# Kernel tuning notes

Measured on AMD Instinct MI355X. Metric: run time of the kernel, lower is better.

Reference implementation:

```python
import jax, jax.numpy as jnp
import numpy as np
from jax import lax


def setup_inputs() -> dict:
    key = jax.random.key(0)
    k1, k2, k3 = jax.random.split(key, 3)
    T, C, H, W = 8, 1024, 64, 64
    features = jax.random.normal(k1, (T, C, H, W), dtype=jnp.float32)
    # Single shared depthwise kernel ([Conv3d]*input_dim shares one module/weight)
    dw_weight = jax.random.normal(k2, (1, 1, 3, 3, 3), dtype=jnp.float32)
    # Pointwise 1x1x1 conv weight [out_c, in_c, 1, 1, 1]
    pw_weight = jax.random.normal(k3, (1024, 1024, 1, 1, 1), dtype=jnp.float32) * 0.03
    return {"features": features, "dw_weight": dw_weight, "pw_weight": pw_weight}


def reference(features, dw_weight, pw_weight):
    T, C, H, W = features.shape
    # torch: expand to [1,T,C,H,W] then torch.reshape to [1,C,T,H,W]
    # (a raw row-major reshape, NOT a transpose) -- replicate exactly.
    x = features.reshape(1, C, T, H, W)
    # Depthwise temporal conv: every channel uses the SAME [1,1,3,3,3] kernel
    # (the torch list is the same Conv3d object repeated). Express as one
    # grouped conv with the kernel tiled over channels.
    w_dw = jnp.tile(dw_weight, (C, 1, 1, 1, 1))  # [C,1,3,3,3]
    y = lax.conv_general_dilated(
        x, w_dw,
        window_strides=(1, 1, 1),
        padding=((1, 1), (1, 1), (1, 1)),
        feature_group_count=C,
        dimension_numbers=("NCDHW", "OIDHW", "NCDHW"),
    )  # [1,C,T,H,W]
    # Pointwise 1x1x1 conv: [C,C] channel-mixing GEMM per voxel.
    z = jnp.einsum("oc,bcthw->bothw", pw_weight[:, :, 0, 0, 0], y)
    # torch: reshape back [1,C,T,H,W] -> [1,T,C,H,W], then squeeze batch dim.
    return z.reshape(1, T, C, H, W)[0]
```

## Files before the change

kernel.cpp:

```cpp
#include <hip/hip_runtime.h>
#include <hip/hip_bf16.h>
#include <stdint.h>

typedef __attribute__((ext_vector_type(8))) short s8v;
typedef __attribute__((ext_vector_type(4))) float f4v;

#define T_TOT 8
#define NSP 32768
#define K_TOT 1024
#define M_TOT 1024

__device__ __forceinline__ unsigned short f2bf(float f) {
  unsigned int u = __float_as_uint(f);
  u += 0x7FFF + ((u >> 16) & 1);
  return (unsigned short)(u >> 16);
}

__global__ __launch_bounds__(256) void dw_kernel(const float* __restrict__ X,
                                                 const float* __restrict__ DW,
                                                 unsigned short* __restrict__ Yn) {
  __shared__ float xin[8 * 18 * 64];
  const int tid = threadIdx.x;
  const int hb  = blockIdx.x;
  const int c   = blockIdx.y;
  const int h0  = hb * 16;

  float kw[27];
#pragma unroll
  for (int j = 0; j < 27; ++j) kw[j] = DW[j];

  const float* Xc = X + (size_t)c * NSP;

#pragma unroll
  for (int i = 0; i < 9; ++i) {
    const int f  = tid + i * 256;
    const int r  = f >> 4;
    const int wq = (f & 15) * 4;
    const int t  = r / 18;
    const int hr = r - t * 18;
    const int hg = h0 - 1 + hr;
    const int hc = min(max(hg, 0), 63);
    float4 v = *(const float4*)(Xc + (t * 64 + hc) * 64 + wq);
    if (hg != hc) v = (float4){0.f, 0.f, 0.f, 0.f};
    *(float4*)&xin[r * 64 + wq] = v;
  }
  __syncthreads();

  const int w  = tid & 63;
  const int hq = tid >> 6;
  const int wl = (w == 0)  ? w : w - 1;
  const int wr = (w == 63) ? w : w + 1;
  const float* bC = &xin[(hq * 4) * 64 + w];
  const float* bL = &xin[(hq * 4) * 64 + wl];
  const float* bR = &xin[(hq * 4) * 64 + wr];
  unsigned short* Yb = Yn + (size_t)c * NSP + (h0 + hq * 4) * 64 + w;

  float a0[4], a1[4], a2[4];
#pragma unroll
  for (int j = 0; j < 4; ++j) { a0[j] = 0.f; a1[j] = 0.f; a2[j] = 0.f; }

#pragma unroll
  for (int tp = 0; tp < 8; ++tp) {
    float v[6][3];
#pragma unroll
    for (int rr = 0; rr < 6; ++rr) {
      const int off = (tp * 18 + rr) * 64;
      float xc = bC[off];
      float xl = bL[off];
      float xr = bR[off];
      if (w == 0)  xl = 0.f;
      if (w == 63) xr = 0.f;
      v[rr][0] = xl; v[rr][1] = xc; v[rr][2] = xr;
    }
#pragma unroll
    for (int j = 0; j < 4; ++j)
#pragma unroll
      for (int kh = 0; kh < 3; ++kh)
#pragma unroll
        for (int kd = 0; kd < 3; ++kd) {
          const float xv = v[j + kh][kd];
          if (tp >= 1) a0[j] += kw[(2 * 3 + kh) * 3 + kd] * xv;
          a1[j] += kw[(1 * 3 + kh) * 3 + kd] * xv;
          if (tp <= 6) a2[j] += kw[(0 * 3 + kh) * 3 + kd] * xv;
        }
    if (tp >= 1) {
      unsigned short* yp = Yb + (size_t)(tp - 1) * 4096;
#pragma unroll
      for (int j = 0; j < 4; ++j) yp[j * 64] = f2bf(a0[j]);
    }
#pragma unroll
    for (int j = 0; j < 4; ++j) { a0[j] = a1[j]; a1[j] = a2[j]; a2[j] = 0.f; }
  }
  {
    unsigned short* yp = Yb + (size_t)7 * 4096;
#pragma unroll
    for (int j = 0; j < 4; ++j) yp[j * 64] = f2bf(a0[j]);
  }
}

__global__ __launch_bounds__(256) void tr_kernel(const unsigned short* __restrict__ Yn,
                                                 unsigned short* __restrict__ Yt) {
  __shared__ unsigned short tb[64][68];
  const int tid = threadIdx.x;
  const int n0  = blockIdx.x * 64;
  const int c0  = blockIdx.y * 64;

#pragma unroll
  for (int i = 0; i < 2; ++i) {
    const int cl = (tid >> 3) + i * 32;
    const int n8 = (tid & 7) * 8;
    const uint4 v = *(const uint4*)(Yn + (size_t)(c0 + cl) * NSP + n0 + n8);
    uint2 lo; lo.x = v.x; lo.y = v.y;
    uint2 hi; hi.x = v.z; hi.y = v.w;
    *(uint2*)&tb[cl][n8]     = lo;
    *(uint2*)&tb[cl][n8 + 4] = hi;
  }
  __syncthreads();

  const int nl = tid >> 2;
  const int cq = tid & 3;
#pragma unroll
  for (int i = 0; i < 2; ++i) {
    const int c8 = cq * 8 + i * 32;
    unsigned int p[4];
#pragma unroll
    for (int j = 0; j < 4; ++j) {
      const unsigned int a = tb[c8 + 2 * j][nl];
      const unsigned int b = tb[c8 + 2 * j + 1][nl];
      p[j] = a | (b << 16);
    }
    uint4 o; o.x = p[0]; o.y = p[1]; o.z = p[2]; o.w = p[3];
    *(uint4*)(Yt + (size_t)(n0 + nl) * 1024 + c0 + c8) = o;
  }
}

__global__ __launch_bounds__(256) void castw_kernel(const float* __restrict__ Wf,
                                                    unsigned short* __restrict__ Wb) {
  const int i = (blockIdx.x * 256 + threadIdx.x) * 4;
  float4 v = *(const float4*)&Wf[i];
  ushort4 o;
  o.x = f2bf(v.x); o.y = f2bf(v.y); o.z = f2bf(v.z); o.w = f2bf(v.w);
  *(ushort4*)&Wb[i] = o;
}

__device__ __forceinline__ void gload_lds16(const void* g, void* lds) {
  __builtin_amdgcn_global_load_lds(
      (const __attribute__((address_space(1))) void*)(uintptr_t)g,
      (__attribute__((address_space(3))) void*)(uintptr_t)lds, 16, 0, 0);
}

__global__ __launch_bounds__(512, 2) void gemm8_kernel(const unsigned short* __restrict__ A,
                                                       const unsigned short* __restrict__ B,
                                                       float* __restrict__ C) {
  __shared__ char smem[131072];
  const int tid  = threadIdx.x;
  const int lane = tid & 63;
  const int wid  = tid >> 6;
  const int wm   = wid >> 2, wn = wid & 3;

  const int wg = (int)blockIdx.x;
  const int lg = (wg & 7) * 64 + (wg >> 3);
  const int bm = lg & 3;
  const int bn = lg >> 2;

  f4v acc[8][4];
#pragma unroll
  for (int i = 0; i < 8; ++i)
#pragma unroll
    for (int j = 0; j < 4; ++j) acc[i][j] = (f4v){0.f, 0.f, 0.f, 0.f};

  const int r  = tid >> 2;
  const int kb = (((tid & 3) ^ ((tid >> 3) & 3)) * 8);
  const unsigned short* ga = A + (size_t)(bm * 256 + r) * K_TOT + kb;
  const unsigned short* gb = B + (size_t)(bn * 256 + r) * K_TOT + kb;
  const int stg = wid * 1024;

#define STAGE_KK(nb, tt, kk)                                                  \
  do {                                                                        \
    const int ko = (tt) * 64 + (kk) * 32;                                     \
    char* ab = smem + (nb) + (kk) * 16384 + stg;                              \
    char* bb = smem + (nb) + 32768 + (kk) * 16384 + stg;                      \
    gload_lds16(ga + ko,                 ab);                                 \
    gload_lds16(ga + 128 * K_TOT + ko,   ab + 8192);                          \
    gload_lds16(gb + ko,                 bb);                                 \
    gload_lds16(gb + 128 * K_TOT + ko,   bb + 8192);                          \
  } while (0)

  const int cph  = ((lane >> 4) ^ ((lane >> 1) & 3)) * 8;
  const int arow = wm * 128 + (lane & 15);
  const int brow = wn * 64  + (lane & 15);

#define PHASE(cu, nx, tt, kk, pf)                                             \
  do {                                                                        \
    const unsigned short* Ac = (const unsigned short*)(smem + (cu));          \
    const unsigned short* Bc = (const unsigned short*)(smem + (cu) + 32768);  \
    s8v av[8], bv[4];                                                         \
    _Pragma("unroll")                                                         \
    for (int nf = 0; nf < 4; ++nf)                                            \
      bv[nf] = *(const s8v*)&Bc[(kk) * 8192 + (brow + nf * 16) * 32 + cph];   \
    _Pragma("unroll")                                                         \
    for (int mf = 0; mf < 8; ++mf)                                            \
      av[mf] = *(const s8v*)&Ac[(kk) * 8192 + (arow + mf * 16) * 32 + cph];   \
    if (pf) STAGE_KK(nx, (tt) + 1, kk);                                       \
    __builtin_amdgcn_s_setprio(1);                                            \
    _Pragma("unroll")                                                         \
    for (int mf = 0; mf < 8; ++mf)                                            \
      _Pragma("unroll")                                                       \
      for (int nf = 0; nf < 4; ++nf)                                          \
        acc[mf][nf] = __builtin_amdgcn_mfma_f32_16x16x32_bf16(                \
            av[mf], bv[nf], acc[mf][nf], 0, 0, 0);                            \
    __builtin_amdgcn_s_setprio(0);                                            \
  } while (0)

  STAGE_KK(0, 0, 0);
  STAGE_KK(0, 0, 1);

  for (int t = 0; t < 15; ++t) {
    const int cu = (t & 1) << 16;
    const int nx = cu ^ 65536;
    asm volatile("s_waitcnt vmcnt(4)" ::: "memory");
    __builtin_amdgcn_s_barrier();
    PHASE(cu, nx, t, 0, true);
    asm volatile("s_waitcnt vmcnt(4)" ::: "memory");
    __builtin_amdgcn_s_barrier();
    PHASE(cu, nx, t, 1, true);
  }
  asm volatile("s_waitcnt vmcnt(0)" ::: "memory");
  __builtin_amdgcn_s_barrier();
  PHASE(65536, 0, 15, 0, false);
  PHASE(65536, 0, 15, 1, false);

#undef PHASE
#undef STAGE_KK

  const int rowq = (lane >> 4) * 4;
  const int colq = lane & 15;
#pragma unroll
  for (int mf = 0; mf < 8; ++mf) {
    const int row0 = bm * 256 + wm * 128 + mf * 16 + rowq;
#pragma unroll
    for (int nf = 0; nf < 4; ++nf) {
      const int col = bn * 256 + wn * 64 + nf * 16 + colq;
      float* cp = C + (size_t)row0 * NSP + col;
#pragma unroll
      for (int j = 0; j < 4; ++j) cp[(size_t)j * NSP] = acc[mf][nf][j];
    }
  }
}

__global__ __launch_bounds__(256) void gemm_nmajor_kernel(const unsigned short* __restrict__ A,
                                                          const unsigned short* __restrict__ B,
                                                          float* __restrict__ C) {
  __shared__ unsigned short As[128][32];
  __shared__ unsigned short Bs[128][40];
  const int tid  = threadIdx.x;
  const int lane = tid & 63;
  const int wv   = tid >> 6;
  const int wr   = wv >> 1, wc = wv & 1;
  const int bn   = blockIdx.x, bm = blockIdx.y;
  const int n0   = bn * 128;

  f4v acc[4][4];
#pragma unroll
  for (int i = 0; i < 4; ++i)
#pragma unroll
    for (int j = 0; j < 4; ++j) acc[i][j] = (f4v){0.f, 0.f, 0.f, 0.f};

  const int r  = tid >> 2;
  const int kb = (tid & 3) * 8;
  const unsigned short* ga0 = A + (size_t)(bm * 128 + r) * K_TOT + kb;
  char* ldsA = (char*)(&As[0][0]) + wv * 1024;
  const int nq4 = (tid >> 3) * 4;
  const int kq4 = (tid & 7) * 4;

  for (int kt = 0; kt < K_TOT; kt += 32) {
    __syncthreads();
    gload_lds16(ga0 + kt,               ldsA);
    gload_lds16(ga0 + 64 * K_TOT + kt,  ldsA + 4096);

    const unsigned short* gB = B + (size_t)(kt + kq4) * NSP + n0 + nq4;
    uint2 L0 = *(const uint2*)(gB);
    uint2 L1 = *(const uint2*)(gB + NSP);
    uint2 L2 = *(const uint2*)(gB + 2 * NSP);
    uint2 L3 = *(const uint2*)(gB + 3 * NSP);
    uint2 W0, W1, W2, W3;
    W0.x = (L0.x & 0xFFFFu) | (L1.x << 16);
    W0.y = (L2.x & 0xFFFFu) | (L3.x << 16);
    W1.x = (L0.x >> 16) | (L1.x & 0xFFFF0000u);
    W1.y = (L2.x >> 16) | (L3.x & 0xFFFF0000u);
    W2.x = (L0.y & 0xFFFFu) | (L1.y << 16);
    W2.y = (L2.y & 0xFFFFu) | (L3.y << 16);
    W3.x = (L0.y >> 16) | (L1.y & 0xFFFF0000u);
    W3.y = (L2.y >> 16) | (L3.y & 0xFFFF0000u);
    *(uint2*)&Bs[nq4 + 0][kq4] = W0;
    *(uint2*)&Bs[nq4 + 1][kq4] = W1;
    *(uint2*)&Bs[nq4 + 2][kq4] = W2;
    *(uint2*)&Bs[nq4 + 3][kq4] = W3;
    __syncthreads();

    s8v a[4], b[4];
#pragma unroll
    for (int mf = 0; mf < 4; ++mf)
      a[mf] = *(const s8v*)&As[wr * 64 + mf * 16 + (lane & 15)][(lane >> 4) * 8];
#pragma unroll
    for (int nf = 0; nf < 4; ++nf)
      b[nf] = *(const s8v*)&Bs[wc * 64 + nf * 16 + (lane & 15)][(lane >> 4) * 8];
#pragma unroll
    for (int mf = 0; mf < 4; ++mf)
#pragma unroll
      for (int nf = 0; nf < 4; ++nf)
        acc[mf][nf] = __builtin_amdgcn_mfma_f32_16x16x32_bf16(a[mf], b[nf], acc[mf][nf], 0, 0, 0);
  }

  const int rowq = (lane >> 4) * 4;
  const int colq = lane & 15;
#pragma unroll
  for (int mf = 0; mf < 4; ++mf) {
    const int row0 = bm * 128 + wr * 64 + mf * 16 + rowq;
#pragma unroll
    for (int nf = 0; nf < 4; ++nf) {
      const int col = n0 + wc * 64 + nf * 16 + colq;
      float* cp = C + (size_t)row0 * NSP + col;
#pragma unroll
      for (int j = 0; j < 4; ++j) cp[(size_t)j * NSP] = acc[mf][nf][j];
    }
  }
}

extern "C" void kernel_launch(void* const* d_in, const int* in_sizes, int n_in,
                              void* d_out, int out_size, void* d_ws, size_t ws_size,
                              hipStream_t stream) {
  const float* feat = (const float*)d_in[0];
  const float* dw   = (const float*)d_in[1];
  const float* pw   = (const float*)d_in[2];
  float* out = (float*)d_out;

  const size_t YBYTES = (size_t)K_TOT * NSP * 2;

  if (ws_size >= 2 * YBYTES) {
    unsigned short* Yt = (unsigned short*)d_ws;
    unsigned short* Yn = (unsigned short*)((char*)d_ws + YBYTES);
    unsigned short* Wb = Yn;
    dw_kernel<<<dim3(4, 1024), dim3(256), 0, stream>>>(feat, dw, Yn);
    tr_kernel<<<dim3(512, 16), dim3(256), 0, stream>>>(Yn, Yt);
    castw_kernel<<<dim3(1024), dim3(256), 0, stream>>>(pw, Wb);
    gemm8_kernel<<<dim3(512), dim3(512), 0, stream>>>(Wb, Yt, out);
  } else {
    unsigned short* Yn = (unsigned short*)d_ws;
    unsigned short* Wb = Yn + (size_t)K_TOT * NSP;
    dw_kernel<<<dim3(4, 1024), dim3(256), 0, stream>>>(feat, dw, Yn);
    castw_kernel<<<dim3(1024), dim3(256), 0, stream>>>(pw, Wb);
    gemm_nmajor_kernel<<<dim3(256, 8), dim3(256), 0, stream>>>(Wb, Yn, out);
  }
}
```

Measured before the change: 151.9 us.

## Split GEMM K-step into four interleaved phases with finer-grained A/B prefetch

Restructures the main GEMM loop so each 64-wide K tile runs as four sub-phases of 16 MFMAs, interleaving LDS fragment reads, separate A and B global-to-LDS prefetches, and barriers. It halves the A-fragment registers and spreads the memory traffic more evenly across the compute, aiming to overlap loads with MFMA work better and lower register pressure. The cost is more barriers per iteration and more delicate vmcnt accounting, which could add stalls or race hazards.

Measured after the change: 152.9 us. About the same (+0.6%).

```diff
diff --git a/kernel.cpp b/kernel.cpp
--- a/kernel.cpp
+++ b/kernel.cpp
@@ -175,63 +175,123 @@
   const unsigned short* gb = B + (size_t)(bn * 256 + r) * K_TOT + kb;
   const int stg = wid * 1024;
 
-#define STAGE_KK(nb, tt, kk)                                                  \
+#define STAGE_A(nb, tt, kk)                                                   \
   do {                                                                        \
     const int ko = (tt) * 64 + (kk) * 32;                                     \
     char* ab = smem + (nb) + (kk) * 16384 + stg;                              \
+    gload_lds16(ga + ko,               ab);                                   \
+    gload_lds16(ga + 128 * K_TOT + ko, ab + 8192);                            \
+  } while (0)
+#define STAGE_B(nb, tt, kk)                                                   \
+  do {                                                                        \
+    const int ko = (tt) * 64 + (kk) * 32;                                     \
     char* bb = smem + (nb) + 32768 + (kk) * 16384 + stg;                      \
-    gload_lds16(ga + ko,                 ab);                                 \
-    gload_lds16(ga + 128 * K_TOT + ko,   ab + 8192);                          \
-    gload_lds16(gb + ko,                 bb);                                 \
-    gload_lds16(gb + 128 * K_TOT + ko,   bb + 8192);                          \
+    gload_lds16(gb + ko,               bb);                                   \
+    gload_lds16(gb + 128 * K_TOT + ko, bb + 8192);                            \
   } while (0)
 
   const int cph  = ((lane >> 4) ^ ((lane >> 1) & 3)) * 8;
   const int arow = wm * 128 + (lane & 15);
   const int brow = wn * 64  + (lane & 15);
 
-#define PHASE(cu, nx, tt, kk, pf)                                             \
+#define MFMA16(mbase, kkreg)                                                  \
   do {                                                                        \
-    const unsigned short* Ac = (const unsigned short*)(smem + (cu));          \
-    const unsigned short* Bc = (const unsigned short*)(smem + (cu) + 32768);  \
-    s8v av[8], bv[4];                                                         \
-    _Pragma("unroll")                                                         \
-    for (int nf = 0; nf < 4; ++nf)                                            \
-      bv[nf] = *(const s8v*)&Bc[(kk) * 8192 + (brow + nf * 16) * 32 + cph];   \
-    _Pragma("unroll")                                                         \
-    for (int mf = 0; mf < 8; ++mf)                                            \
-      av[mf] = *(const s8v*)&Ac[(kk) * 8192 + (arow + mf * 16) * 32 + cph];   \
-    if (pf) STAGE_KK(nx, (tt) + 1, kk);                                       \
     __builtin_amdgcn_s_setprio(1);                                            \
     _Pragma("unroll")                                                         \
-    for (int mf = 0; mf < 8; ++mf)                                            \
+    for (int mf = 0; mf < 4; ++mf)                                            \
       _Pragma("unroll")                                                       \
       for (int nf = 0; nf < 4; ++nf)                                          \
-        acc[mf][nf] = __builtin_amdgcn_mfma_f32_16x16x32_bf16(                \
-            av[mf], bv[nf], acc[mf][nf], 0, 0, 0);                            \
+        acc[(mbase) + mf][nf] = __builtin_amdgcn_mfma_f32_16x16x32_bf16(      \
+            av[mf], bv[nf], acc[(mbase) + mf][nf], 0, 0, 0);                  \
     __builtin_amdgcn_s_setprio(0);                                            \
   } while (0)
 
-  STAGE_KK(0, 0, 0);
-  STAGE_KK(0, 0, 1);
+  STAGE_A(0, 0, 0);
+  STAGE_B(0, 0, 0);
+  STAGE_A(0, 0, 1);
+  STAGE_B(0, 0, 1);
+  asm volatile("s_waitcnt vmcnt(4)" ::: "memory");
+  __builtin_amdgcn_s_barrier();
 
   for (int t = 0; t < 15; ++t) {
     const int cu = (t & 1) << 16;
     const int nx = cu ^ 65536;
+    const unsigned short* Ac = (const unsigned short*)(smem + cu);
+    const unsigned short* Bc = (const unsigned short*)(smem + cu + 32768);
+    s8v av[4], bv[4];
+
+#pragma unroll
+    for (int nf = 0; nf < 4; ++nf)
+      bv[nf] = *(const s8v*)&Bc[(brow + nf * 16) * 32 + cph];
+#pragma unroll
+    for (int mf = 0; mf < 4; ++mf)
+      av[mf] = *(const s8v*)&Ac[(arow + mf * 16) * 32 + cph];
+    STAGE_A(nx, t + 1, 0);
+    __builtin_amdgcn_s_barrier();
+    MFMA16(0, 0);
+
+#pragma unroll
+    for (int mf = 0; mf < 4; ++mf)
+      av[mf] = *(const s8v*)&Ac[(arow + (mf + 4) * 16) * 32 + cph];
+    STAGE_B(nx, t + 1, 0);
     asm volatile("s_waitcnt vmcnt(4)" ::: "memory");
     __builtin_amdgcn_s_barrier();
-    PHASE(cu, nx, t, 0, true);
+    MFMA16(4, 0);
+
+#pragma unroll
+    for (int nf = 0; nf < 4; ++nf)
+      bv[nf] = *(const s8v*)&Bc[8192 + (brow + nf * 16) * 32 + cph];
+#pragma unroll
+    for (int mf = 0; mf < 4; ++mf)
+      av[mf] = *(const s8v*)&Ac[8192 + (arow + mf * 16) * 32 + cph];
+    STAGE_A(nx, t + 1, 1);
+    __builtin_amdgcn_s_barrier();
+    MFMA16(0, 1);
+
+#pragma unroll
+    for (int mf = 0; mf < 4; ++mf)
+      av[mf] = *(const s8v*)&Ac[8192 + (arow + (mf + 4) * 16) * 32 + cph];
+    STAGE_B(nx, t + 1, 1);
     asm volatile("s_waitcnt vmcnt(4)" ::: "memory");
     __builtin_amdgcn_s_barrier();
-    PHASE(cu, nx, t, 1, true);
-  }
-  asm volatile("s_waitcnt vmcnt(0)" ::: "memory");
-  __builtin_amdgcn_s_barrier();
-  PHASE(65536, 0, 15, 0, false);
-  PHASE(65536, 0, 15, 1, false);
-
-#undef PHASE
-#undef STAGE_KK
+    MFMA16(4, 1);
+  }
+
+  {
+    const unsigned short* Ac = (const unsigned short*)(smem + 65536);
+    const unsigned short* Bc = (const unsigned short*)(smem + 65536 + 32768);
+    s8v av[4], bv[4];
+#pragma unroll
+    for (int nf = 0; nf < 4; ++nf)
+      bv[nf] = *(const s8v*)&Bc[(brow + nf * 16) * 32 + cph];
+#pragma unroll
+    for (int mf = 0; mf < 4; ++mf)
+      av[mf] = *(const s8v*)&Ac[(arow + mf * 16) * 32 + cph];
+    __builtin_amdgcn_s_barrier();
+    MFMA16(0, 0);
+#pragma unroll
+    for (int mf = 0; mf < 4; ++mf)
+      av[mf] = *(const s8v*)&Ac[(arow + (mf + 4) * 16) * 32 + cph];
+    asm volatile("s_waitcnt vmcnt(0)" ::: "memory");
+    __builtin_amdgcn_s_barrier();
+    MFMA16(4, 0);
+#pragma unroll
+    for (int nf = 0; nf < 4; ++nf)
+      bv[nf] = *(const s8v*)&Bc[8192 + (brow + nf * 16) * 32 + cph];
+#pragma unroll
+    for (int mf = 0; mf < 4; ++mf)
+      av[mf] = *(const s8v*)&Ac[8192 + (arow + mf * 16) * 32 + cph];
+    __builtin_amdgcn_s_barrier();
+    MFMA16(0, 1);
+#pragma unroll
+    for (int mf = 0; mf < 4; ++mf)
+      av[mf] = *(const s8v*)&Ac[8192 + (arow + (mf + 4) * 16) * 32 + cph];
+    MFMA16(4, 1);
+  }
+
+#undef MFMA16
+#undef STAGE_A
+#undef STAGE_B
 
   const int rowq = (lane >> 4) * 4;
   const int colq = lane & 15;
```

## Fuse transpose and weight cast into depthwise kernel with 8-channel interleaved layout

Applied to the files above, without the earlier changes.

The depthwise conv kernel now handles 8 channels per block and writes its output as 8-channel bf16 chunks per spatial position (a channel-group-major layout), so the separate transpose kernel is dropped. The weight cast is folded into extra blocks of the same launch. The GEMM B loads are re-addressed to read 16-byte chunks from the new layout. This removes a full read/write pass over the 64MB intermediate and two kernel launches. In exchange, the depthwise kernel has a large register footprint (held[8][4][4]) and only 512 blocks, which may lower occupancy.

Measured after the change: 149.8 us. No clear change (-1.4%).

```diff
diff --git a/kernel.cpp b/kernel.cpp
--- a/kernel.cpp
+++ b/kernel.cpp
@@ -16,35 +16,33 @@
   return (unsigned short)(u >> 16);
 }
 
-__global__ __launch_bounds__(256) void dw_kernel(const float* __restrict__ X,
-                                                 const float* __restrict__ DW,
-                                                 unsigned short* __restrict__ Yn) {
+__global__ __launch_bounds__(256, 2) void dw3_kernel(const float* __restrict__ X,
+                                                     const float* __restrict__ DW,
+                                                     unsigned short* __restrict__ Yn8,
+                                                     const float* __restrict__ Wf,
+                                                     unsigned short* __restrict__ Wb) {
+  if (blockIdx.x == 4) {
+    const int base = blockIdx.y * 8192;
+#pragma unroll
+    for (int it = 0; it < 8; ++it) {
+      const int i = base + (it * 256 + (int)threadIdx.x) * 4;
+      float4 v = *(const float4*)&Wf[i];
+      ushort4 o;
+      o.x = f2bf(v.x); o.y = f2bf(v.y); o.z = f2bf(v.z); o.w = f2bf(v.w);
+      *(ushort4*)&Wb[i] = o;
+    }
+    return;
+  }
+
   __shared__ float xin[8 * 18 * 64];
   const int tid = threadIdx.x;
   const int hb  = blockIdx.x;
-  const int c   = blockIdx.y;
+  const int cg  = blockIdx.y;
   const int h0  = hb * 16;
 
   float kw[27];
 #pragma unroll
   for (int j = 0; j < 27; ++j) kw[j] = DW[j];
-
-  const float* Xc = X + (size_t)c * NSP;
-
-#pragma unroll
-  for (int i = 0; i < 9; ++i) {
-    const int f  = tid + i * 256;
-    const int r  = f >> 4;
-    const int wq = (f & 15) * 4;
-    const int t  = r / 18;
-    const int hr = r - t * 18;
-    const int hg = h0 - 1 + hr;
-    const int hc = min(max(hg, 0), 63);
-    float4 v = *(const float4*)(Xc + (t * 64 + hc) * 64 + wq);
-    if (hg != hc) v = (float4){0.f, 0.f, 0.f, 0.f};
-    *(float4*)&xin[r * 64 + wq] = v;
-  }
-  __syncthreads();
 
   const int w  = tid & 63;
   const int hq = tid >> 6;
@@ -53,94 +51,90 @@
   const float* bC = &xin[(hq * 4) * 64 + w];
   const float* bL = &xin[(hq * 4) * 64 + wl];
   const float* bR = &xin[(hq * 4) * 64 + wr];
-  unsigned short* Yb = Yn + (size_t)c * NSP + (h0 + hq * 4) * 64 + w;
-
-  float a0[4], a1[4], a2[4];
-#pragma unroll
-  for (int j = 0; j < 4; ++j) { a0[j] = 0.f; a1[j] = 0.f; a2[j] = 0.f; }
-
-#pragma unroll
-  for (int tp = 0; tp < 8; ++tp) {
-    float v[6][3];
-#pragma unroll
-    for (int rr = 0; rr < 6; ++rr) {
-      const int off = (tp * 18 + rr) * 64;
-      float xc = bC[off];
-      float xl = bL[off];
-      float xr = bR[off];
-      if (w == 0)  xl = 0.f;
-      if (w == 63) xr = 0.f;
-      v[rr][0] = xl; v[rr][1] = xc; v[rr][2] = xr;
-    }
-#pragma unroll
-    for (int j = 0; j < 4; ++j)
-#pragma unroll
-      for (int kh = 0; kh < 3; ++kh)
-#pragma unroll
-        for (int kd = 0; kd < 3; ++kd) {
-          const float xv = v[j + kh][kd];
-          if (tp >= 1) a0[j] += kw[(2 * 3 + kh) * 3 + kd] * xv;
-          a1[j] += kw[(1 * 3 + kh) * 3 + kd] * xv;
-          if (tp <= 6) a2[j] += kw[(0 * 3 + kh) * 3 + kd] * xv;
+
+  unsigned int held[8][4][4];
+
+#pragma unroll
+  for (int c = 0; c < 8; ++c) {
+    const float* Xc = X + (size_t)(cg * 8 + c) * NSP;
+
+#pragma unroll
+    for (int i = 0; i < 9; ++i) {
+      const int f  = tid + i * 256;
+      const int r  = f >> 4;
+      const int wq = (f & 15) * 4;
+      const int t  = r / 18;
+      const int hr = r - t * 18;
+      const int hg = h0 - 1 + hr;
+      const int hc = min(max(hg, 0), 63);
+      float4 v = *(const float4*)(Xc + (t * 64 + hc) * 64 + wq);
+      if (hg != hc) v = (float4){0.f, 0.f, 0.f, 0.f};
+      *(float4*)&xin[r * 64 + wq] = v;
+    }
+    __syncthreads();
+
+    float a0[4], a1[4], a2[4];
+#pragma unroll
+    for (int j = 0; j < 4; ++j) { a0[j] = 0.f; a1[j] = 0.f; a2[j] = 0.f; }
+
+#pragma unroll
+    for (int tp = 0; tp < 8; ++tp) {
+      float v[6][3];
+#pragma unroll
+      for (int rr = 0; rr < 6; ++rr) {
+        const int off = (tp * 18 + rr) * 64;
+        float xc = bC[off];
+        float xl = bL[off];
+        float xr = bR[off];
+        if (w == 0)  xl = 0.f;
+        if (w == 63) xr = 0.f;
+        v[rr][0] = xl; v[rr][1] = xc; v[rr][2] = xr;
+      }
+#pragma unroll
+      for (int j = 0; j < 4; ++j)
+#pragma unroll
+        for (int kh = 0; kh < 3; ++kh)
+#pragma unroll
+          for (int kd = 0; kd < 3; ++kd) {
+            const float xv = v[j + kh][kd];
+            if (tp >= 1) a0[j] += kw[(2 * 3 + kh) * 3 + kd] * xv;
+            a1[j] += kw[(1 * 3 + kh) * 3 + kd] * xv;
+            if (tp <= 6) a2[j] += kw[(0 * 3 + kh) * 3 + kd] * xv;
+          }
+      if (tp >= 1) {
+        const int to = tp - 1;
+#pragma unroll
+        for (int j = 0; j < 4; ++j) {
+          const unsigned int b = f2bf(a0[j]);
+          if (c & 1) held[to][j][c >> 1] |= (b << 16);
+          else       held[to][j][c >> 1] = b;
         }
-    if (tp >= 1) {
-      unsigned short* yp = Yb + (size_t)(tp - 1) * 4096;
-#pragma unroll
-      for (int j = 0; j < 4; ++j) yp[j * 64] = f2bf(a0[j]);
-    }
-#pragma unroll
-    for (int j = 0; j < 4; ++j) { a0[j] = a1[j]; a1[j] = a2[j]; a2[j] = 0.f; }
-  }
-  {
-    unsigned short* yp = Yb + (size_t)7 * 4096;
-#pragma unroll
-    for (int j = 0; j < 4; ++j) yp[j * 64] = f2bf(a0[j]);
-  }
-}
-
-__global__ __launch_bounds__(256) void tr_kernel(const unsigned short* __restrict__ Yn,
-                                                 unsigned short* __restrict__ Yt) {
-  __shared__ unsigned short tb[64][68];
-  const int tid = threadIdx.x;
-  const int n0  = blockIdx.x * 64;
-  const int c0  = blockIdx.y * 64;
-
-#pragma unroll
-  for (int i = 0; i < 2; ++i) {
-    const int cl = (tid >> 3) + i * 32;
-    const int n8 = (tid & 7) * 8;
-    const uint4 v = *(const uint4*)(Yn + (size_t)(c0 + cl) * NSP + n0 + n8);
-    uint2 lo; lo.x = v.x; lo.y = v.y;
-    uint2 hi; hi.x = v.z; hi.y = v.w;
-    *(uint2*)&tb[cl][n8]     = lo;
-    *(uint2*)&tb[cl][n8 + 4] = hi;
-  }
-  __syncthreads();
-
-  const int nl = tid >> 2;
-  const int cq = tid & 3;
-#pragma unroll
-  for (int i = 0; i < 2; ++i) {
-    const int c8 = cq * 8 + i * 32;
-    unsigned int p[4];
+      }
+#pragma unroll
+      for (int j = 0; j < 4; ++j) { a0[j] = a1[j]; a1[j] = a2[j]; a2[j] = 0.f; }
+    }
+    {
+#pragma unroll
+      for (int j = 0; j < 4; ++j) {
+        const unsigned int b = f2bf(a0[j]);
+        if (c & 1) held[7][j][c >> 1] |= (b << 16);
+        else       held[7][j][c >> 1] = b;
+      }
+    }
+    __syncthreads();
+  }
+
+  const size_t nb = (size_t)cg * NSP;
+#pragma unroll
+  for (int t = 0; t < 8; ++t)
 #pragma unroll
     for (int j = 0; j < 4; ++j) {
-      const unsigned int a = tb[c8 + 2 * j][nl];
-      const unsigned int b = tb[c8 + 2 * j + 1][nl];
-      p[j] = a | (b << 16);
-    }
-    uint4 o; o.x = p[0]; o.y = p[1]; o.z = p[2]; o.w = p[3];
-    *(uint4*)(Yt + (size_t)(n0 + nl) * 1024 + c0 + c8) = o;
-  }
-}
-
-__global__ __launch_bounds__(256) void castw_kernel(const float* __restrict__ Wf,
-                                                    unsigned short* __restrict__ Wb) {
-  const int i = (blockIdx.x * 256 + threadIdx.x) * 4;
-  float4 v = *(const float4*)&Wf[i];
-  ushort4 o;
-  o.x = f2bf(v.x); o.y = f2bf(v.y); o.z = f2bf(v.z); o.w = f2bf(v.w);
-  *(ushort4*)&Wb[i] = o;
+      const int n = t * 4096 + (h0 + hq * 4 + j) * 64 + w;
+      uint4 o;
+      o.x = held[t][j][0]; o.y = held[t][j][1];
+      o.z = held[t][j][2]; o.w = held[t][j][3];
+      *(uint4*)&Yn8[(nb + (size_t)n) * 8] = o;
+    }
 }
 
 __device__ __forceinline__ void gload_lds16(const void* g, void* lds) {
@@ -150,7 +144,7 @@
 }
 
 __global__ __launch_bounds__(512, 2) void gemm8_kernel(const unsigned short* __restrict__ A,
-                                                       const unsigned short* __restrict__ B,
+                                                       const unsigned short* __restrict__ Yn8,
                                                        float* __restrict__ C) {
   __shared__ char smem[131072];
   const int tid  = threadIdx.x;
@@ -169,21 +163,22 @@
 #pragma unroll
     for (int j = 0; j < 4; ++j) acc[i][j] = (f4v){0.f, 0.f, 0.f, 0.f};
 
-  const int r  = tid >> 2;
-  const int kb = (((tid & 3) ^ ((tid >> 3) & 3)) * 8);
-  const unsigned short* ga = A + (size_t)(bm * 256 + r) * K_TOT + kb;
-  const unsigned short* gb = B + (size_t)(bn * 256 + r) * K_TOT + kb;
+  const int r    = tid >> 2;
+  const int cswz = (tid & 3) ^ ((tid >> 3) & 3);
+  const unsigned short* ga  = A + (size_t)(bm * 256 + r) * K_TOT + cswz * 8;
+  const unsigned short* gbb = Yn8 + ((size_t)cswz * NSP + (size_t)(bn * 256 + r)) * 8;
   const int stg = wid * 1024;
 
 #define STAGE_KK(nb, tt, kk)                                                  \
   do {                                                                        \
     const int ko = (tt) * 64 + (kk) * 32;                                     \
+    const size_t bko = (size_t)((tt) * 8 + (kk) * 4) * NSP * 8;               \
     char* ab = smem + (nb) + (kk) * 16384 + stg;                              \
     char* bb = smem + (nb) + 32768 + (kk) * 16384 + stg;                      \
     gload_lds16(ga + ko,                 ab);                                 \
     gload_lds16(ga + 128 * K_TOT + ko,   ab + 8192);                          \
-    gload_lds16(gb + ko,                 bb);                                 \
-    gload_lds16(gb + 128 * K_TOT + ko,   bb + 8192);                          \
+    gload_lds16(gbb + bko,               bb);                                 \
+    gload_lds16(gbb + bko + 128 * 8,     bb + 8192);                          \
   } while (0)
 
   const int cph  = ((lane >> 4) ^ ((lane >> 1) & 3)) * 8;
@@ -248,85 +243,6 @@
   }
 }
 
-__global__ __launch_bounds__(256) void gemm_nmajor_kernel(const unsigned short* __restrict__ A,
-                                                          const unsigned short* __restrict__ B,
-                                                          float* __restrict__ C) {
-  __shared__ unsigned short As[128][32];
-  __shared__ unsigned short Bs[128][40];
-  const int tid  = threadIdx.x;
-  const int lane = tid & 63;
-  const int wv   = tid >> 6;
-  const int wr   = wv >> 1, wc = wv & 1;
-  const int bn   = blockIdx.x, bm = blockIdx.y;
-  const int n0   = bn * 128;
-
-  f4v acc[4][4];
-#pragma unroll
-  for (int i = 0; i < 4; ++i)
-#pragma unroll
-    for (int j = 0; j < 4; ++j) acc[i][j] = (f4v){0.f, 0.f, 0.f, 0.f};
-
-  const int r  = tid >> 2;
-  const int kb = (tid & 3) * 8;
-  const unsigned short* ga0 = A + (size_t)(bm * 128 + r) * K_TOT + kb;
-  char* ldsA = (char*)(&As[0][0]) + wv * 1024;
-  const int nq4 = (tid >> 3) * 4;
-  const int kq4 = (tid & 7) * 4;
-
-  for (int kt = 0; kt < K_TOT; kt += 32) {
-    __syncthreads();
-    gload_lds16(ga0 + kt,               ldsA);
-    gload_lds16(ga0 + 64 * K_TOT + kt,  ldsA + 4096);
-
-    const unsigned short* gB = B + (size_t)(kt + kq4) * NSP + n0 + nq4;
-    uint2 L0 = *(const uint2*)(gB);
-    uint2 L1 = *(const uint2*)(gB + NSP);
-    uint2 L2 = *(const uint2*)(gB + 2 * NSP);
-    uint2 L3 = *(const uint2*)(gB + 3 * NSP);
-    uint2 W0, W1, W2, W3;
-    W0.x = (L0.x & 0xFFFFu) | (L1.x << 16);
-    W0.y = (L2.x & 0xFFFFu) | (L3.x << 16);
-    W1.x = (L0.x >> 16) | (L1.x & 0xFFFF0000u);
-    W1.y = (L2.x >> 16) | (L3.x & 0xFFFF0000u);
-    W2.x = (L0.y & 0xFFFFu) | (L1.y << 16);
-    W2.y = (L2.y & 0xFFFFu) | (L3.y << 16);
-    W3.x = (L0.y >> 16) | (L1.y & 0xFFFF0000u);
-    W3.y = (L2.y >> 16) | (L3.y & 0xFFFF0000u);
-    *(uint2*)&Bs[nq4 + 0][kq4] = W0;
-    *(uint2*)&Bs[nq4 + 1][kq4] = W1;
-    *(uint2*)&Bs[nq4 + 2][kq4] = W2;
-    *(uint2*)&Bs[nq4 + 3][kq4] = W3;
-    __syncthreads();
-
-    s8v a[4], b[4];
-#pragma unroll
-    for (int mf = 0; mf < 4; ++mf)
-      a[mf] = *(const s8v*)&As[wr * 64 + mf * 16 + (lane & 15)][(lane >> 4) * 8];
-#pragma unroll
-    for (int nf = 0; nf < 4; ++nf)
-      b[nf] = *(const s8v*)&Bs[wc * 64 + nf * 16 + (lane & 15)][(lane >> 4) * 8];
-#pragma unroll
-    for (int mf = 0; mf < 4; ++mf)
-#pragma unroll
-      for (int nf = 0; nf < 4; ++nf)
-        acc[mf][nf] = __builtin_amdgcn_mfma_f32_16x16x32_bf16(a[mf], b[nf], acc[mf][nf], 0, 0, 0);
-  }
-
-  const int rowq = (lane >> 4) * 4;
-  const int colq = lane & 15;
-#pragma unroll
-  for (int mf = 0; mf < 4; ++mf) {
-    const int row0 = bm * 128 + wr * 64 + mf * 16 + rowq;
-#pragma unroll
-    for (int nf = 0; nf < 4; ++nf) {
-      const int col = n0 + wc * 64 + nf * 16 + colq;
-      float* cp = C + (size_t)row0 * NSP + col;
-#pragma unroll
-      for (int j = 0; j < 4; ++j) cp[(size_t)j * NSP] = acc[mf][nf][j];
-    }
-  }
-}
-
 extern "C" void kernel_launch(void* const* d_in, const int* in_sizes, int n_in,
                               void* d_out, int out_size, void* d_ws, size_t ws_size,
                               hipStream_t stream) {
@@ -335,21 +251,9 @@
   const float* pw   = (const float*)d_in[2];
   float* out = (float*)d_out;
 
-  const size_t YBYTES = (size_t)K_TOT * NSP * 2;
-
-  if (ws_size >= 2 * YBYTES) {
-    unsigned short* Yt = (unsigned short*)d_ws;
-    unsigned short* Yn = (unsigned short*)((char*)d_ws + YBYTES);
-    unsigned short* Wb = Yn;
-    dw_kernel<<<dim3(4, 1024), dim3(256), 0, stream>>>(feat, dw, Yn);
-    tr_kernel<<<dim3(512, 16), dim3(256), 0, stream>>>(Yn, Yt);
-    castw_kernel<<<dim3(1024), dim3(256), 0, stream>>>(pw, Wb);
-    gemm8_kernel<<<dim3(512), dim3(512), 0, stream>>>(Wb, Yt, out);
-  } else {
-    unsigned short* Yn = (unsigned short*)d_ws;
-    unsigned short* Wb = Yn + (size_t)K_TOT * NSP;
-    dw_kernel<<<dim3(4, 1024), dim3(256), 0, stream>>>(feat, dw, Yn);
-    castw_kernel<<<dim3(1024), dim3(256), 0, stream>>>(pw, Wb);
-    gemm_nmajor_kernel<<<dim3(256, 8), dim3(256), 0, stream>>>(Wb, Yn, out);
-  }
-}
+  unsigned short* Yn8 = (unsigned short*)d_ws;
+  unsigned short* Wb  = Yn8 + (size_t)K_TOT * NSP;
+
+  dw3_kernel<<<dim3(5, 128), dim3(256), 0, stream>>>(feat, dw, Yn8, pw, Wb);
+  gemm8_kernel<<<dim3(512), dim3(512), 0, stream>>>(Wb, Yn8, out);
+}
```

## Fold weight cast into depthwise kernel and use channel-octet layout for GEMM B

Applied to the files above, without the earlier changes.

The bf16 weight cast now runs as an extra column of blocks inside the depthwise kernel, which removes one launch. The full N-major transpose is replaced by a lighter transpose into a [C/8][N][8] layout, so each 16-byte GEMM load gets 8 consecutive channels for one voxel. The GEMM B-operand staging addresses are rewritten for this layout. B-side global loads now stride across channel groups by NSP*8, which may change coalescing and cache behaviour, and the workspace needs an extra weight buffer.

Result: no change. 149.4 us (-1.7%).

```diff
diff --git a/kernel.cpp b/kernel.cpp
--- a/kernel.cpp
+++ b/kernel.cpp
@@ -18,7 +18,18 @@
 
 __global__ __launch_bounds__(256) void dw_kernel(const float* __restrict__ X,
                                                  const float* __restrict__ DW,
-                                                 unsigned short* __restrict__ Yn) {
+                                                 unsigned short* __restrict__ Yn,
+                                                 const float* __restrict__ Wf,
+                                                 unsigned short* __restrict__ Wb) {
+  if (blockIdx.x == 4) {
+    const int i = (blockIdx.y * 256 + threadIdx.x) * 4;
+    float4 v = *(const float4*)&Wf[i];
+    ushort4 o;
+    o.x = f2bf(v.x); o.y = f2bf(v.y); o.z = f2bf(v.z); o.w = f2bf(v.w);
+    *(ushort4*)&Wb[i] = o;
+    return;
+  }
+
   __shared__ float xin[8 * 18 * 64];
   const int tid = threadIdx.x;
   const int hb  = blockIdx.x;
@@ -98,49 +109,33 @@
   }
 }
 
-__global__ __launch_bounds__(256) void tr_kernel(const unsigned short* __restrict__ Yn,
-                                                 unsigned short* __restrict__ Yt) {
-  __shared__ unsigned short tb[64][68];
+__global__ __launch_bounds__(256) void tr8_kernel(const unsigned short* __restrict__ Yn,
+                                                  unsigned short* __restrict__ Yn8) {
+  __shared__ unsigned short tb[8][1032];
   const int tid = threadIdx.x;
-  const int n0  = blockIdx.x * 64;
-  const int c0  = blockIdx.y * 64;
-
-#pragma unroll
-  for (int i = 0; i < 2; ++i) {
-    const int cl = (tid >> 3) + i * 32;
-    const int n8 = (tid & 7) * 8;
-    const uint4 v = *(const uint4*)(Yn + (size_t)(c0 + cl) * NSP + n0 + n8);
-    uint2 lo; lo.x = v.x; lo.y = v.y;
-    uint2 hi; hi.x = v.z; hi.y = v.w;
-    *(uint2*)&tb[cl][n8]     = lo;
-    *(uint2*)&tb[cl][n8 + 4] = hi;
+  const int n0  = blockIdx.x * 1024;
+  const int cg  = blockIdx.y;
+
+#pragma unroll
+  for (int i = 0; i < 4; ++i) {
+    const int f   = tid + i * 256;
+    const int row = f >> 7;
+    const int col = (f & 127) * 8;
+    const uint4 v = *(const uint4*)&Yn[(size_t)(cg * 8 + row) * NSP + n0 + col];
+    *(uint4*)&tb[row][col] = v;
   }
   __syncthreads();
 
-  const int nl = tid >> 2;
-  const int cq = tid & 3;
-#pragma unroll
-  for (int i = 0; i < 2; ++i) {
-    const int c8 = cq * 8 + i * 32;
-    unsigned int p[4];
-#pragma unroll
-    for (int j = 0; j < 4; ++j) {
-      const unsigned int a = tb[c8 + 2 * j][nl];
-      const unsigned int b = tb[c8 + 2 * j + 1][nl];
-      p[j] = a | (b << 16);
-    }
-    uint4 o; o.x = p[0]; o.y = p[1]; o.z = p[2]; o.w = p[3];
-    *(uint4*)(Yt + (size_t)(n0 + nl) * 1024 + c0 + c8) = o;
-  }
-}
-
-__global__ __launch_bounds__(256) void castw_kernel(const float* __restrict__ Wf,
-                                                    unsigned short* __restrict__ Wb) {
-  const int i = (blockIdx.x * 256 + threadIdx.x) * 4;
-  float4 v = *(const float4*)&Wf[i];
-  ushort4 o;
-  o.x = f2bf(v.x); o.y = f2bf(v.y); o.z = f2bf(v.z); o.w = f2bf(v.w);
-  *(ushort4*)&Wb[i] = o;
+#pragma unroll
+  for (int i = 0; i < 4; ++i) {
+    const int n = tid + i * 256;
+    uint4 o;
+    o.x = (unsigned)tb[0][n] | ((unsigned)tb[1][n] << 16);
+    o.y = (unsigned)tb[2][n] | ((unsigned)tb[3][n] << 16);
+    o.z = (unsigned)tb[4][n] | ((unsigned)tb[5][n] << 16);
+    o.w = (unsigned)tb[6][n] | ((unsigned)tb[7][n] << 16);
+    *(uint4*)&Yn8[((size_t)cg * NSP + n0 + n) * 8] = o;
+  }
 }
 
 __device__ __forceinline__ void gload_lds16(const void* g, void* lds) {
@@ -150,7 +145,7 @@
 }
 
 __global__ __launch_bounds__(512, 2) void gemm8_kernel(const unsigned short* __restrict__ A,
-                                                       const unsigned short* __restrict__ B,
+                                                       const unsigned short* __restrict__ Yn8,
                                                        float* __restrict__ C) {
   __shared__ char smem[131072];
   const int tid  = threadIdx.x;
@@ -169,21 +164,22 @@
 #pragma unroll
     for (int j = 0; j < 4; ++j) acc[i][j] = (f4v){0.f, 0.f, 0.f, 0.f};
 
-  const int r  = tid >> 2;
-  const int kb = (((tid & 3) ^ ((tid >> 3) & 3)) * 8);
-  const unsigned short* ga = A + (size_t)(bm * 256 + r) * K_TOT + kb;
-  const unsigned short* gb = B + (size_t)(bn * 256 + r) * K_TOT + kb;
+  const int r    = tid >> 2;
+  const int cswz = (tid & 3) ^ ((tid >> 3) & 3);
+  const unsigned short* ga  = A + (size_t)(bm * 256 + r) * K_TOT + cswz * 8;
+  const unsigned short* gbb = Yn8 + ((size_t)cswz * NSP + (size_t)(bn * 256 + r)) * 8;
   const int stg = wid * 1024;
 
 #define STAGE_KK(nb, tt, kk)                                                  \
   do {                                                                        \
     const int ko = (tt) * 64 + (kk) * 32;                                     \
+    const size_t bko = (size_t)((tt) * 8 + (kk) * 4) * NSP * 8;               \
     char* ab = smem + (nb) + (kk) * 16384 + stg;                              \
     char* bb = smem + (nb) + 32768 + (kk) * 16384 + stg;                      \
     gload_lds16(ga + ko,                 ab);                                 \
     gload_lds16(ga + 128 * K_TOT + ko,   ab + 8192);                          \
-    gload_lds16(gb + ko,                 bb);                                 \
-    gload_lds16(gb + 128 * K_TOT + ko,   bb + 8192);                          \
+    gload_lds16(gbb + bko,               bb);                                 \
+    gload_lds16(gbb + bko + 128 * 8,     bb + 8192);                          \
   } while (0)
 
   const int cph  = ((lane >> 4) ^ ((lane >> 1) & 3)) * 8;
@@ -336,20 +332,19 @@
   float* out = (float*)d_out;
 
   const size_t YBYTES = (size_t)K_TOT * NSP * 2;
-
-  if (ws_size >= 2 * YBYTES) {
-    unsigned short* Yt = (unsigned short*)d_ws;
-    unsigned short* Yn = (unsigned short*)((char*)d_ws + YBYTES);
-    unsigned short* Wb = Yn;
-    dw_kernel<<<dim3(4, 1024), dim3(256), 0, stream>>>(feat, dw, Yn);
-    tr_kernel<<<dim3(512, 16), dim3(256), 0, stream>>>(Yn, Yt);
-    castw_kernel<<<dim3(1024), dim3(256), 0, stream>>>(pw, Wb);
-    gemm8_kernel<<<dim3(512), dim3(512), 0, stream>>>(Wb, Yt, out);
+  const size_t WBYTES = (size_t)M_TOT * K_TOT * 2;
+
+  if (ws_size >= 2 * YBYTES + WBYTES) {
+    unsigned short* Yn  = (unsigned short*)d_ws;
+    unsigned short* Yn8 = (unsigned short*)((char*)d_ws + YBYTES);
+    unsigned short* Wb  = (unsigned short*)((char*)d_ws + 2 * YBYTES);
+    dw_kernel<<<dim3(5, 1024), dim3(256), 0, stream>>>(feat, dw, Yn, pw, Wb);
+    tr8_kernel<<<dim3(32, 128), dim3(256), 0, stream>>>(Yn, Yn8);
+    gemm8_kernel<<<dim3(512), dim3(512), 0, stream>>>(Wb, Yn8, out);
   } else {
     unsigned short* Yn = (unsigned short*)d_ws;
     unsigned short* Wb = Yn + (size_t)K_TOT * NSP;
-    dw_kernel<<<dim3(4, 1024), dim3(256), 0, stream>>>(feat, dw, Yn);
-    castw_kernel<<<dim3(1024), dim3(256), 0, stream>>>(pw, Wb);
+    dw_kernel<<<dim3(5, 1024), dim3(256), 0, stream>>>(feat, dw, Yn, pw, Wb);
     gemm_nmajor_kernel<<<dim3(256, 8), dim3(256), 0, stream>>>(Wb, Yn, out);
   }
 }
```
